# Optimization experiments

Measured on AMD Instinct MI355X. Metric: run time of the kernel, lower is better.

The kernel has to match this reference:

```python
import jax, jax.numpy as jnp
import numpy as np

B, S, H = 32, 1024, 1024
W, K = 128, 6
NUM_HEADS = 16


def setup_inputs() -> dict:
    key = jax.random.key(0)
    k1, k2 = jax.random.split(key, 2)
    token_embeddings = jax.random.normal(k1, (B, S, H), dtype=jnp.float32)
    # nn.MultiheadAttention packed in_proj (q,k,v). v / out_proj never affect the
    # module output (attn_output is discarded), but we keep full-size params.
    in_proj_weight = jax.random.normal(k2, (3 * H, H), dtype=jnp.float32) * (1.0 / np.sqrt(H))
    in_proj_bias = jnp.zeros((3 * H,), dtype=jnp.float32)
    # Build ragged word->subtoken map as padded [B, W, K] indices + validity mask.
    # Words occupy disjoint contiguous slots (stride S//W = 8 >= K), matching the
    # disjointness the tokenizer guarantees in get_subtok_map.
    rng = np.random.default_rng(0)
    lengths = rng.integers(2, K + 1, size=(B, W))  # each kept word has >=2 subtokens
    stride = S // W
    base = (np.arange(W) * stride)[None, :, None] + np.arange(K)[None, None, :]
    base = np.broadcast_to(base, (B, W, K))
    mask = np.arange(K)[None, None, :] < lengths[:, :, None]
    idx = np.where(mask, base, 0)
    return {
        "token_embeddings": token_embeddings,
        "in_proj_weight": in_proj_weight,
        "in_proj_bias": in_proj_bias,
        "subtok_idx": jnp.asarray(idx, dtype=jnp.int32),
        "subtok_mask": jnp.asarray(mask),
        "num_heads": NUM_HEADS,
    }


def _merge(token_embeddings, in_proj_weight, in_proj_bias, subtok_idx, subtok_mask, num_heads):
    Bv, Sv, Hv = token_embeddings.shape
    Wv, Kv = subtok_idx.shape[1], subtok_idx.shape[2]
    hd = Hv // num_heads
    dtype = token_embeddings.dtype
    maskf = subtok_mask.astype(dtype)
    b_idx = jnp.arange(Bv)[:, None, None]
    sub = token_embeddings[b_idx, subtok_idx]                      # [B,W,K,H] gather
    x = (sub * maskf[..., None]).reshape(Bv * Wv, Kv, Hv)          # zero-padded groups
    # q,k projections (v / out_proj do not influence returned embeddings)
    qk = x @ in_proj_weight[: 2 * Hv].T + in_proj_bias[: 2 * Hv]
    q, k = qk[..., :Hv], qk[..., Hv:]
    q = q.reshape(-1, Kv, num_heads, hd).transpose(0, 2, 1, 3)     # [L,nh,K,hd]
    k = k.reshape(-1, Kv, num_heads, hd).transpose(0, 2, 1, 3)
    scores = jnp.einsum('lnqd,lnkd->lnqk', q, k) / jnp.asarray(np.sqrt(hd), dtype)
    m = maskf.reshape(-1, Kv)
    pair = m[:, :, None] * m[:, None, :]                           # [L,K,K] 0/1 float mask
    # torch adds float attn_mask to scores (it does NOT -inf mask here) -- faithful
    scores = scores + pair[:, None]
    attn = jax.nn.softmax(scores, axis=-1)
    w_mean = attn.mean(axis=1)                                     # avg over heads (need_weights)
    contrib = (pair * w_mean).sum(axis=1)                          # sum over query dim
    contrib = contrib / (contrib.sum(axis=-1, keepdims=True) + 1e-8)
    contrib = contrib.reshape(Bv, Wv, Kv)                          # zero at invalid k
    unified = jnp.einsum('bwkh,bwk->bwh', sub, contrib)
    # zero ALL subtoken positions of each word, then write merged vector at the
    # first subtoken index (equivalent to the torch in-place per-word loop since
    # word index sets are disjoint). Column Sv is a discard slot for padding.
    safe_idx = jnp.where(subtok_mask, subtok_idx, Sv)
    keep = jnp.ones((Bv, Sv + 1), dtype=dtype)
    keep = keep.at[b_idx, safe_idx].set(0.0)
    out = token_embeddings * keep[:, :Sv, None]
    out = jnp.concatenate([out, jnp.zeros((Bv, 1, Hv), dtype)], axis=1)
    first_idx = jnp.where(subtok_mask[:, :, 0], subtok_idx[:, :, 0], Sv)
    out = out.at[jnp.arange(Bv)[:, None], first_idx].set(unified)
    return out[:, :Sv]


def reference(token_embeddings, in_proj_weight, in_proj_bias, subtok_idx, subtok_mask, num_heads):
    return _merge(token_embeddings, in_proj_weight, in_proj_bias, subtok_idx, subtok_mask, num_heads)
```

## Files before the change

### kernel.cpp

```cpp
#include <hip/hip_runtime.h>
#include <hip/hip_bf16.h>
#include <stdint.h>
#include <stddef.h>

#define Bdim  32
#define Sdim  1024
#define Hdim  1024
#define Wdim  128
#define Ktok  6
#define NHEAD 16
#define HDdim 64
#define Lgrp  (Bdim*Wdim)
#define Mrows (Lgrp*Ktok)
#define Ncols (2*Hdim)
#define CVTROWS (Mrows + Ncols)

#define BMg 256
#define BNg 256
#define BKg 64
#define NKT (Hdim/BKg)

typedef __attribute__((ext_vector_type(8))) short short8;
typedef __attribute__((ext_vector_type(4))) short short4_t;
typedef __attribute__((ext_vector_type(4))) float floatx4;
typedef __hip_bfloat16 bf16_t;

typedef unsigned int u32_g __attribute__((address_space(1)));
typedef unsigned int u32_l __attribute__((address_space(3)));

__device__ __forceinline__ void gld_lds16(const void* g, void* l) {
    __builtin_amdgcn_global_load_lds((const u32_g*)g, (u32_l*)l, 16, 0, 0);
}

__device__ __forceinline__ float b2f(short s) {
    union { float f; unsigned u; } x; x.u = ((unsigned)(unsigned short)s) << 16; return x.f;
}

__device__ __forceinline__ short8 cvt8(const float4 lo, const float4 hi) {
    union { short8 s; bf16_t h[8]; } u;
    u.h[0] = __float2bfloat16(lo.x); u.h[1] = __float2bfloat16(lo.y);
    u.h[2] = __float2bfloat16(lo.z); u.h[3] = __float2bfloat16(lo.w);
    u.h[4] = __float2bfloat16(hi.x); u.h[5] = __float2bfloat16(hi.y);
    u.h[6] = __float2bfloat16(hi.z); u.h[7] = __float2bfloat16(hi.w);
    return u.s;
}

__device__ __forceinline__ int lds_ro(int row, int col) {
    const int sub = ((row >> 4) << 1) | (col >> 5);
    const int c   = (col & 31) ^ (((row >> 3) & 1) << 4);
    return (sub << 10) | ((row & 15) << 6) | (c << 1);
}
__device__ __forceinline__ void stg_map(int p, int& row, int& col) {
    const int r16 = (p >> 6) & 15;
    int c = (p >> 1) & 31;
    c ^= ((r16 >> 3) & 1) << 4;
    row = ((p >> 11) << 4) | r16;
    col = (((p >> 10) & 1) << 5) | c;
}

__global__ void zero_zf(unsigned int* __restrict__ zf)
{
    zf[blockIdx.x * 256 + threadIdx.x] = 0u;
}

__global__ void gather_cvt(const float* __restrict__ TE, const float* __restrict__ Wt,
                           const int* __restrict__ sidx,
                           bf16_t* __restrict__ Xa, bf16_t* __restrict__ Wb,
                           unsigned char* __restrict__ zflag)
{
    const int r = blockIdx.x;
    const int t = threadIdx.x;
    const float* src;
    bf16_t* dst;
    if (r < Mrows) {
        const int id = sidx[r];
        const int b  = r / (Wdim*Ktok);
        src = TE + ((size_t)b*Sdim + id)*Hdim;
        dst = Xa + (size_t)r*Hdim;
        if (t == 0 && (r % Ktok) >= 1 && id != 0) zflag[b*Sdim + id] = 1;
    } else {
        src = Wt + (size_t)(r - Mrows)*Hdim;
        dst = Wb + (size_t)(r - Mrows)*Hdim;
    }
    const float4 v = *(const float4*)(src + t*4);
    union { short4_t s; bf16_t h[4]; } u;
    u.h[0] = __float2bfloat16(v.x); u.h[1] = __float2bfloat16(v.y);
    u.h[2] = __float2bfloat16(v.z); u.h[3] = __float2bfloat16(v.w);
    *(short4_t*)(dst + t*4) = u.s;
}

__global__ __launch_bounds__(512, 2) void gemm_8ph(
    const bf16_t* __restrict__ Xa, const bf16_t* __restrict__ Wb,
    const float* __restrict__ bias, bf16_t* __restrict__ Cq)
{
    __shared__ __align__(16) char lds[2][2][2][16384];
    const int tid  = threadIdx.x;
    const int lane = tid & 63;
    const int wv   = tid >> 6;
    const int wr   = wv >> 2;
    const int wc   = wv & 3;
    const int fr   = lane & 15;
    const int fq   = lane >> 4;

    const int cpx  = gridDim.x >> 3;
    const int orig = blockIdx.x;
    const int swz  = (orig & 7) * cpx + (orig >> 3);
    const int tileM = (swz >> 3) * BMg;
    const int tileN = (swz & 7) * BNg;

    int r0, c0, r1, c1;
    stg_map(tid * 16, r0, c0);
    stg_map(8192 + tid * 16, r1, c1);

    const bf16_t* srcA = Xa + (size_t)tileM * Hdim;
    const bf16_t* srcB = Wb + (size_t)tileN * Hdim;

    int aoff[4][2], boff[2][2];
    #pragma unroll
    for (int mi = 0; mi < 4; mi++)
        #pragma unroll
        for (int ks = 0; ks < 2; ks++)
            aoff[mi][ks] = lds_ro(wr*64 + mi*16 + fr, ks*32 + fq*8);
    #pragma unroll
    for (int ni = 0; ni < 2; ni++)
        #pragma unroll
        for (int ks = 0; ks < 2; ks++)
            boff[ni][ks] = lds_ro(wc*32 + ni*16 + fr, ks*32 + fq*8);

    short8 a[4][2], b[2][2];
    floatx4 acc[2][2][4][2] = {};

#define STAGE(bufi, isB, half, kt) do { \
        const bf16_t* _s = (isB) ? srcB : srcA; \
        char* _d = &lds[(bufi)][(isB)][(half)][0]; \
        const int _kb = (kt) * BKg; \
        gld_lds16(_s + (size_t)((half)*128 + r0) * Hdim + _kb + c0, _d + tid*16); \
        gld_lds16(_s + (size_t)((half)*128 + r1) * Hdim + _kb + c1, _d + 8192 + tid*16); \
    } while (0)

#define LDAf(bufi, qr) do { \
        const char* _sA = &lds[(bufi)][0][(qr)][0]; \
        _Pragma("unroll") \
        for (int mi = 0; mi < 4; mi++) { \
            a[mi][0] = *(const short8*)(const void*)(_sA + aoff[mi][0]); \
            a[mi][1] = *(const short8*)(const void*)(_sA + aoff[mi][1]); \
        } \
    } while (0)

#define LDBf(bufi, qc) do { \
        const char* _sB = &lds[(bufi)][1][(qc)][0]; \
        _Pragma("unroll") \
        for (int ni = 0; ni < 2; ni++) { \
            b[ni][0] = *(const short8*)(const void*)(_sB + boff[ni][0]); \
            b[ni][1] = *(const short8*)(const void*)(_sB + boff[ni][1]); \
        } \
    } while (0)

#define MMA(qr, qc) do { \
        __builtin_amdgcn_s_setprio(1); \
        _Pragma("unroll") \
        for (int mi = 0; mi < 4; mi++) \
            _Pragma("unroll") \
            for (int ni = 0; ni < 2; ni++) { \
                acc[qr][qc][mi][ni] = __builtin_amdgcn_mfma_f32_16x16x32_bf16( \
                    a[mi][0], b[ni][0], acc[qr][qc][mi][ni], 0, 0, 0); \
                acc[qr][qc][mi][ni] = __builtin_amdgcn_mfma_f32_16x16x32_bf16( \
                    a[mi][1], b[ni][1], acc[qr][qc][mi][ni], 0, 0, 0); \
            } \
        __builtin_amdgcn_s_setprio(0); \
    } while (0)

    STAGE(0, 0, 0, 0);
    STAGE(0, 1, 0, 0);
    STAGE(0, 0, 1, 0);
    STAGE(0, 1, 1, 0);
    STAGE(1, 0, 0, 1);
    STAGE(1, 1, 1, 1);
    asm volatile("s_waitcnt vmcnt(4)" ::: "memory");
    __builtin_amdgcn_s_barrier();

    for (int u = 0; u < NKT; ++u) {
        const int bf = u & 1;
        const int nb = bf ^ 1;
        LDAf(bf, 0);
        LDBf(bf, 0);
        if (u + 1 < NKT) STAGE(nb, 0, 1, u + 1);
        MMA(0, 0);
        LDBf(bf, 1);
        if (u + 1 < NKT) STAGE(nb, 1, 0, u + 1);
        MMA(0, 1);
        __builtin_amdgcn_s_barrier();
        LDAf(bf, 1);
        if (u + 2 < NKT) { STAGE(bf, 0, 0, u + 2); STAGE(bf, 1, 1, u + 2); }
        MMA(1, 1);
        LDBf(bf, 0);
        MMA(1, 0);
        if (u + 2 < NKT)      asm volatile("s_waitcnt vmcnt(4)" ::: "memory");
        else if (u + 1 < NKT) asm volatile("s_waitcnt vmcnt(0)" ::: "memory");
        __builtin_amdgcn_s_barrier();
    }

    #pragma unroll
    for (int qr = 0; qr < 2; qr++)
      #pragma unroll
      for (int qc = 0; qc < 2; qc++)
        #pragma unroll
        for (int ni = 0; ni < 2; ni++) {
            const int col = tileN + qc*128 + wc*32 + ni*16 + fr;
            const float bv = bias[col];
            #pragma unroll
            for (int mi = 0; mi < 4; mi++)
              #pragma unroll
              for (int j = 0; j < 4; j++) {
                const int row = tileM + qr*128 + wr*64 + mi*16 + fq*4 + j;
                Cq[(size_t)row * Ncols + col] = __float2bfloat16(acc[qr][qc][mi][ni][j] + bv);
              }
        }
#undef STAGE
#undef LDAf
#undef LDBf
#undef MMA
}

__global__ __launch_bounds__(256, 2) void gemm_qk(
    const float* __restrict__ TE, const float* __restrict__ Wt,
    const float* __restrict__ bias, const int* __restrict__ sidx,
    bf16_t* __restrict__ Cq)
{
    __shared__ __align__(16) bf16_t As[128*32];
    __shared__ __align__(16) bf16_t Bs[128*32];
    const int tid  = threadIdx.x;
    const int wv   = tid >> 6;
    const int lane = tid & 63;
    const int tileM = blockIdx.x * 128;
    const int tileN = blockIdx.y * 128;

    const int r0 = wv*32 + (lane>>2);
    const int r1 = r0 + 16;
    const int c8 = (lane&3)*8;

    const int m0 = tileM + r0;
    const int m1 = tileM + r1;
    const float* pA0 = TE + ((size_t)(m0/768)*Sdim + sidx[m0])*Hdim + c8;
    const float* pA1 = TE + ((size_t)(m1/768)*Sdim + sidx[m1])*Hdim + c8;
    const float* pB0 = Wt + (size_t)(tileN + r0)*Hdim + c8;
    const float* pB1 = Wt + (size_t)(tileN + r1)*Hdim + c8;
    bf16_t* lA0 = &As[r0*32 + c8];
    bf16_t* lA1 = &As[r1*32 + c8];
    bf16_t* lB0 = &Bs[r0*32 + c8];
    bf16_t* lB1 = &Bs[r1*32 + c8];

    const int wm = (wv & 1)*64;
    const int wn = (wv >> 1)*64;
    const int fr = lane & 15;
    const int fq = lane >> 4;

    floatx4 acc[4][4] = {};

    for (int k0 = 0; k0 < Hdim; k0 += 32) {
        const float4 a0l = *(const float4*)(pA0 + k0);
        const float4 a0h = *(const float4*)(pA0 + k0 + 4);
        const float4 a1l = *(const float4*)(pA1 + k0);
        const float4 a1h = *(const float4*)(pA1 + k0 + 4);
        const float4 b0l = *(const float4*)(pB0 + k0);
        const float4 b0h = *(const float4*)(pB0 + k0 + 4);
        const float4 b1l = *(const float4*)(pB1 + k0);
        const float4 b1h = *(const float4*)(pB1 + k0 + 4);
        *(short8*)(void*)lA0 = cvt8(a0l, a0h);
        *(short8*)(void*)lA1 = cvt8(a1l, a1h);
        *(short8*)(void*)lB0 = cvt8(b0l, b0h);
        *(short8*)(void*)lB1 = cvt8(b1l, b1h);
        __syncthreads();
        short8 a[4], b[4];
        #pragma unroll
        for (int mi = 0; mi < 4; mi++)
            a[mi] = *(const short8*)(const void*)&As[(wm + mi*16 + fr)*32 + fq*8];
        #pragma unroll
        for (int ni = 0; ni < 4; ni++)
            b[ni] = *(const short8*)(const void*)&Bs[(wn + ni*16 + fr)*32 + fq*8];
        #pragma unroll
        for (int mi = 0; mi < 4; mi++)
            #pragma unroll
            for (int ni = 0; ni < 4; ni++)
                acc[mi][ni] = __builtin_amdgcn_mfma_f32_16x16x32_bf16(
                    a[mi], b[ni], acc[mi][ni], 0, 0, 0);
        __syncthreads();
    }

    #pragma unroll
    for (int ni = 0; ni < 4; ni++) {
        const int col = tileN + wn + ni*16 + fr;
        const float bv = bias[col];
        #pragma unroll
        for (int mi = 0; mi < 4; mi++) {
            #pragma unroll
            for (int r = 0; r < 4; r++) {
                const int row = tileM + wm + mi*16 + fq*4 + r;
                Cq[(size_t)row * Ncols + col] = __float2bfloat16(acc[mi][ni][r] + bv);
            }
        }
    }
}

__global__ void copy_te(const uint4* __restrict__ src, uint4* __restrict__ dst,
                        const unsigned char* __restrict__ zflag, int n)
{
    int i = blockIdx.x * blockDim.x + threadIdx.x;
    const int stride = gridDim.x * blockDim.x;
    const uint4 z = {0u, 0u, 0u, 0u};
    for (; i < n; i += stride) {
        if (zflag != nullptr && zflag[i >> 8]) dst[i] = z;
        else dst[i] = src[i];
    }
}

__global__ __launch_bounds__(256) void attn_merge(
    const float* __restrict__ TE, const bf16_t* __restrict__ Cq,
    const float* __restrict__ bias, const int* __restrict__ sidx,
    float* __restrict__ out, int zero_rows)
{
    __shared__ __align__(16) bf16_t qk[Ktok][Ncols];
    __shared__ float sc[NHEAD][Ktok][Ktok];
    __shared__ float cN[Ktok];
    __shared__ int   validS[Ktok];

    const int g   = blockIdx.x;
    const int b   = g >> 7;
    const int w   = g & (Wdim - 1);
    const int tid = threadIdx.x;

    if (tid < Ktok) {
        const int id = sidx[g*Ktok + tid];
        validS[tid] = (id != 0) || (w == 0 && tid == 0);
    }
    __syncthreads();

    int valid[Ktok], idxv[Ktok];
    #pragma unroll
    for (int kk = 0; kk < Ktok; kk++) { valid[kk] = validS[kk]; idxv[kk] = sidx[g*Ktok + kk]; }

    #pragma unroll
    for (int it = 0; it < Ktok; it++) {
        if (valid[it]) {
            *(short8*)(void*)&qk[it][tid*8] =
                *(const short8*)(const void*)&Cq[(size_t)(g*Ktok + it)*Ncols + tid*8];
        } else {
            const float4 lo = *(const float4*)(bias + tid*8);
            const float4 hi = *(const float4*)(bias + tid*8 + 4);
            *(short8*)(void*)&qk[it][tid*8] = cvt8(lo, hi);
        }
    }
    __syncthreads();

    for (int t = tid; t < NHEAD*Ktok*Ktok; t += 256) {
        const int n = t / (Ktok*Ktok);
        const int pr = t % (Ktok*Ktok);
        const int i = pr / Ktok, j = pr % Ktok;
        const bf16_t* qp = &qk[i][n*HDdim];
        const bf16_t* kp = &qk[j][Hdim + n*HDdim];
        float dot = 0.f;
        #pragma unroll
        for (int c = 0; c < 8; c++) {
            const short8 q8 = *(const short8*)(const void*)(qp + c*8);
            const short8 k8 = *(const short8*)(const void*)(kp + c*8);
            #pragma unroll
            for (int e = 0; e < 8; e++) dot += b2f(q8[e]) * b2f(k8[e]);
        }
        sc[n][i][j] = dot * 0.125f + ((valid[i] && valid[j]) ? 1.0f : 0.0f);
    }
    __syncthreads();

    if (tid < NHEAD*Ktok) {
        const int n = tid / Ktok, i = tid % Ktok;
        float mx = -1e30f;
        #pragma unroll
        for (int j = 0; j < Ktok; j++) mx = fmaxf(mx, sc[n][i][j]);
        float e[Ktok], sum = 0.f;
        #pragma unroll
        for (int j = 0; j < Ktok; j++) { e[j] = __expf(sc[n][i][j] - mx); sum += e[j]; }
        const float inv = 1.0f / sum;
        #pragma unroll
        for (int j = 0; j < Ktok; j++) sc[n][i][j] = e[j] * inv;
    }
    __syncthreads();

    if (tid == 0) {
        float cb[Ktok], tot = 0.f;
        #pragma unroll
        for (int j = 0; j < Ktok; j++) cb[j] = 0.f;
        #pragma unroll
        for (int i = 0; i < Ktok; i++) {
            if (!valid[i]) continue;
            #pragma unroll
            for (int j = 0; j < Ktok; j++) {
                if (!valid[j]) continue;
                float s = 0.f;
                #pragma unroll
                for (int n = 0; n < NHEAD; n++) s += sc[n][i][j];
                cb[j] += s * (1.0f/NHEAD);
            }
        }
        #pragma unroll
        for (int j = 0; j < Ktok; j++) tot += cb[j];
        const float inv = 1.0f / (tot + 1e-8f);
        #pragma unroll
        for (int j = 0; j < Ktok; j++) cN[j] = cb[j] * inv;
    }
    __syncthreads();

    float cw[Ktok];
    #pragma unroll
    for (int kk = 0; kk < Ktok; kk++) cw[kk] = cN[kk];

    const int c4 = tid * 4;
    const size_t rowOut = ((size_t)b*Sdim + idxv[0]) * Hdim;
    float4 u = {0.f, 0.f, 0.f, 0.f};
    #pragma unroll
    for (int kk = 0; kk < Ktok; kk++) {
        const float4 v = *(const float4*)(TE + ((size_t)b*Sdim + idxv[kk])*Hdim + c4);
        u.x += cw[kk]*v.x; u.y += cw[kk]*v.y; u.z += cw[kk]*v.z; u.w += cw[kk]*v.w;
    }
    *(float4*)(out + rowOut + c4) = u;

    if (zero_rows) {
        const float4 z = {0.f, 0.f, 0.f, 0.f};
        #pragma unroll
        for (int kk = 1; kk < Ktok; kk++) {
            if (valid[kk]) {
                *(float4*)(out + ((size_t)b*Sdim + idxv[kk])*Hdim + c4) = z;
            }
        }
    }
}

extern "C" void kernel_launch(void* const* d_in, const int* in_sizes, int n_in,
                              void* d_out, int out_size, void* d_ws, size_t ws_size,
                              hipStream_t stream)
{
    (void)in_sizes; (void)n_in; (void)out_size;
    const float* TE   = (const float*)d_in[0];
    const float* Wt   = (const float*)d_in[1];
    const float* bias = (const float*)d_in[2];
    const int*   sidx = (const int*)d_in[3];
    float*  out  = (float*)d_out;

    const size_t CQ_BYTES = (size_t)Mrows * Ncols * 2;
    const size_t XA_BYTES = (size_t)Mrows * Hdim * 2;
    const size_t WB_BYTES = (size_t)Ncols * Hdim * 2;
    const size_t ZF_BYTES = (size_t)Bdim * Sdim;
    bf16_t* Cq = (bf16_t*)d_ws;
    bf16_t* Xa = (bf16_t*)((char*)d_ws + CQ_BYTES);
    bf16_t* Wb = (bf16_t*)((char*)d_ws + CQ_BYTES + XA_BYTES);
    unsigned char* zf = (unsigned char*)((char*)d_ws + CQ_BYTES + XA_BYTES + WB_BYTES);

    if (ws_size >= CQ_BYTES + XA_BYTES + WB_BYTES + ZF_BYTES) {
        zero_zf<<<ZF_BYTES/1024, 256, 0, stream>>>((unsigned int*)zf);
        gather_cvt<<<CVTROWS, 256, 0, stream>>>(TE, Wt, sidx, Xa, Wb, zf);
        gemm_8ph<<<dim3((Mrows/BMg)*(Ncols/BNg)), dim3(512), 0, stream>>>(Xa, Wb, bias, Cq);
        copy_te<<<4096, 256, 0, stream>>>((const uint4*)TE, (uint4*)d_out, zf,
                                          (Bdim*Sdim*Hdim)/4);
        attn_merge<<<Lgrp, 256, 0, stream>>>(TE, Cq, bias, sidx, out, 0);
    } else {
        dim3 gg(Mrows/128, Ncols/128);
        gemm_qk<<<gg, dim3(256), 0, stream>>>(TE, Wt, bias, sidx, Cq);
        copy_te<<<4096, 256, 0, stream>>>((const uint4*)TE, (uint4*)d_out, nullptr,
                                          (Bdim*Sdim*Hdim)/4);
        attn_merge<<<Lgrp, 256, 0, stream>>>(TE, Cq, bias, sidx, out, 1);
    }
}
```

Measured before the change: 400.9 us.

## Vectorize GEMM epilogue stores, skip first-subtoken copies, pad merge LDS rows

Swaps the MFMA operand order so each lane's accumulator holds four consecutive output columns. The epilogue can then load bias as a float4 and write packed 4-wide bf16 stores instead of scalar strided stores. The zero-flag buffer gains a third state marking each word's first subtoken, so the copy kernel skips rows that the merge kernel will overwrite anyway. It also pads the attention-merge shared qk rows to reduce bank conflicts. The risk is correctness: first-subtoken rows are no longer written by copy, so any word the merge kernel does not overwrite would keep stale data.

```diff
diff --git a/kernel.cpp b/kernel.cpp
--- a/kernel.cpp
+++ b/kernel.cpp
@@ -75,9 +75,13 @@
     if (r < Mrows) {
         const int id = sidx[r];
         const int b  = r / (Wdim*Ktok);
+        if (t == 0) {
+            const int k = r % Ktok;
+            if (k == 0)       zflag[b*Sdim + id] = 2;
+            else if (id != 0) zflag[b*Sdim + id] = 1;
+        }
         src = TE + ((size_t)b*Sdim + id)*Hdim;
         dst = Xa + (size_t)r*Hdim;
-        if (t == 0 && (r % Ktok) >= 1 && id != 0) zflag[b*Sdim + id] = 1;
     } else {
         src = Wt + (size_t)(r - Mrows)*Hdim;
         dst = Wb + (size_t)(r - Mrows)*Hdim;
@@ -163,9 +167,9 @@
             _Pragma("unroll") \
             for (int ni = 0; ni < 2; ni++) { \
                 acc[qr][qc][mi][ni] = __builtin_amdgcn_mfma_f32_16x16x32_bf16( \
-                    a[mi][0], b[ni][0], acc[qr][qc][mi][ni], 0, 0, 0); \
+                    b[ni][0], a[mi][0], acc[qr][qc][mi][ni], 0, 0, 0); \
                 acc[qr][qc][mi][ni] = __builtin_amdgcn_mfma_f32_16x16x32_bf16( \
-                    a[mi][1], b[ni][1], acc[qr][qc][mi][ni], 0, 0, 0); \
+                    b[ni][1], a[mi][1], acc[qr][qc][mi][ni], 0, 0, 0); \
             } \
         __builtin_amdgcn_s_setprio(0); \
     } while (0)
@@ -206,15 +210,18 @@
       for (int qc = 0; qc < 2; qc++)
         #pragma unroll
         for (int ni = 0; ni < 2; ni++) {
-            const int col = tileN + qc*128 + wc*32 + ni*16 + fr;
-            const float bv = bias[col];
+            const int n0 = tileN + qc*128 + wc*32 + ni*16 + fq*4;
+            const float4 bv = *(const float4*)(bias + n0);
             #pragma unroll
-            for (int mi = 0; mi < 4; mi++)
-              #pragma unroll
-              for (int j = 0; j < 4; j++) {
-                const int row = tileM + qr*128 + wr*64 + mi*16 + fq*4 + j;
-                Cq[(size_t)row * Ncols + col] = __float2bfloat16(acc[qr][qc][mi][ni][j] + bv);
-              }
+            for (int mi = 0; mi < 4; mi++) {
+                const int m = tileM + qr*128 + wr*64 + mi*16 + fr;
+                union { short4_t s; bf16_t h[4]; } p;
+                p.h[0] = __float2bfloat16(acc[qr][qc][mi][ni][0] + bv.x);
+                p.h[1] = __float2bfloat16(acc[qr][qc][mi][ni][1] + bv.y);
+                p.h[2] = __float2bfloat16(acc[qr][qc][mi][ni][2] + bv.z);
+                p.h[3] = __float2bfloat16(acc[qr][qc][mi][ni][3] + bv.w);
+                *(short4_t*)&Cq[(size_t)m * Ncols + n0] = p.s;
+            }
         }
 #undef STAGE
 #undef LDAf
@@ -309,8 +316,9 @@
     const int stride = gridDim.x * blockDim.x;
     const uint4 z = {0u, 0u, 0u, 0u};
     for (; i < n; i += stride) {
-        if (zflag != nullptr && zflag[i >> 8]) dst[i] = z;
-        else dst[i] = src[i];
+        const unsigned char f = zflag ? zflag[i >> 8] : (unsigned char)0;
+        if (f == 0)      dst[i] = src[i];
+        else if (f == 1) dst[i] = z;
     }
 }
 
@@ -319,7 +327,7 @@
     const float* __restrict__ bias, const int* __restrict__ sidx,
     float* __restrict__ out, int zero_rows)
 {
-    __shared__ __align__(16) bf16_t qk[Ktok][Ncols];
+    __shared__ __align__(16) bf16_t qk[Ktok][Ncols + 8];
     __shared__ float sc[NHEAD][Ktok][Ktok];
     __shared__ float cN[Ktok];
     __shared__ int   validS[Ktok];
```

After: 404.2 us. No clear change (+0.8%).
